# Kernel optimization log

Measured on AMD Instinct MI355X. Metric: run time of the kernel, lower is better.

## Reference

```python
import jax, jax.numpy as jnp
import numpy as np

N_COMP = 8
N_BASIS = 16
N_FEATURES = 64
N_CAT = 8
N_CONT = 56
N_UNIQUE = 100
BATCH = 32768
T0, T1 = 0.0, 10.0
SEP = 1e-3  # constants.MIN_TRANSITION_POINT_SEP
SIGNS = np.array([1.0, -1.0, 1.0, -1.0, 1.0, -1.0, 1.0, -1.0], dtype=np.float32)
CONT_IDX = np.arange(N_CONT)
CAT_IDX = np.arange(N_CONT, N_FEATURES)


def _offset():
    # torch_inverse_softplus(avg_interval_per_feature)
    v = (T1 - T0) / N_COMP / (N_FEATURES + 1)
    return float(np.log(np.exp(v) - 1.0))


def setup_inputs():
    key = jax.random.key(0)
    ks = jax.random.split(key, 11)
    off = _offset()
    B = jax.random.normal(ks[0], (BATCH, N_CONT, N_BASIS), jnp.float32)
    codes = jax.random.randint(ks[1], (BATCH, N_CAT), 0, N_UNIQUE)
    B_cat = jax.nn.one_hot(codes, N_UNIQUE, dtype=jnp.float32).reshape(BATCH, N_CAT * N_UNIQUE)
    Wh = jax.random.normal(ks[2], (N_BASIS, N_CONT, N_COMP), jnp.float32) + off
    Wh_cat = jax.random.normal(ks[3], (N_CAT, N_UNIQUE, N_COMP), jnp.float32) + off
    bh = jax.random.normal(ks[4], (N_COMP,), jnp.float32) + off
    Wv = jax.random.normal(ks[5], (N_BASIS, N_CONT, N_COMP), jnp.float32)
    Wv_cat = jax.random.normal(ks[6], (N_CAT, N_UNIQUE, N_COMP), jnp.float32)
    bv = jax.random.normal(ks[7], (N_COMP,), jnp.float32)
    Wic = jax.random.normal(ks[8], (N_BASIS, N_CONT, 1), jnp.float32)
    Wic_cat = jax.random.normal(ks[9], (N_CAT, N_UNIQUE, 1), jnp.float32)
    bic = jax.random.normal(ks[10], (1,), jnp.float32)
    return {"B": B, "B_cat": B_cat, "Wh": Wh, "Wh_cat": Wh_cat, "bh": bh,
            "Wv": Wv, "Wv_cat": Wv_cat, "bv": bv,
            "Wic": Wic, "Wic_cat": Wic_cat, "bic": bic}


def _calculate_gams(B, B_cat, W, W_cat, bias, positive):
    # continuous: per-feature small matmul  (b,i,k) x (k,i,c) -> (b,c,i)
    cont = jnp.einsum('bik,kic->bci', B, W)
    # categorical: one-hot gather expressed as blockwise matmul  (b,f,n) x (f,n,c) -> (b,c,f)
    cat = jnp.einsum('bfn,fnc->bcf', B_cat.reshape(B.shape[0], N_CAT, N_UNIQUE), W_cat)
    c = W.shape[2]
    out = jnp.zeros((B.shape[0], c, N_FEATURES + 1), dtype=B.dtype)
    out = out.at[:, :, CONT_IDX].set(cont)
    out = out.at[:, :, CAT_IDX].set(cat)
    out = out.at[:, :, -1].set(bias[None, :])
    return jax.nn.softplus(out) if positive else out


def reference(B, B_cat, Wh, Wh_cat, bh, Wv, Wv_cat, bv, Wic, Wic_cat, bic):
    H = _calculate_gams(B, B_cat, Wh, Wh_cat, bh, True)      # (b, n_comp, n_feat+1)
    V = _calculate_gams(B, B_cat, Wv, Wv_cat, bv, True)      # (b, n_comp, n_feat+1)
    IC = _calculate_gams(B, B_cat, Wic, Wic_cat, bic, False)  # (b, 1, n_feat+1)
    b = B.shape[0]
    signs = jnp.asarray(SIGNS)
    h_sum = H.sum(-1)   # (b, n_comp) per-segment horizontal increments
    v_sum = V.sum(-1)
    sep = SEP * jnp.arange(1, N_COMP + 1, dtype=B.dtype)
    # sequential cumulative build == prefix sums over the composition axis
    t = jnp.concatenate([jnp.full((b, 1), T0, B.dtype),
                         T0 + jnp.cumsum(h_sum, axis=1) + sep], axis=1)  # (b, n_comp+1)
    x0 = IC.sum(-1)     # (b, 1)
    x = jnp.concatenate([x0, x0 + jnp.cumsum(signs * v_sum, axis=1)], axis=1)
    # bounded composition: clamp the last horizontal coordinate
    t = t.at[:, -1].set(jnp.maximum(t[:, -2] + SEP, T1))
    return jnp.stack([t, x], axis=-1)  # (b, n_comp+1, 2)
```

## Files before the change

### kernel.cpp

```cpp
#include <hip/hip_runtime.h>

#define NCOMP 8
#define NCONT 56
#define NCAT 8
#define NU 100
#define NROWS 32768
#define SEPC 1e-3f
#define T1F 10.0f

typedef __fp16 f16x2 __attribute__((ext_vector_type(2)));
typedef _Float16 h2arith __attribute__((ext_vector_type(2)));

#define HSTRIDE 17
#define ICSTRIDE 3

union H8 { f16x2 h2[4]; float4 f4; };

__device__ __forceinline__ float sp(float x) {
    return 0.69314718f * __builtin_amdgcn_logf(1.0f + __builtin_amdgcn_exp2f(x * 1.44269504f));
}

__device__ __forceinline__ f16x2 pkrtz(float a, float b) {
    return __builtin_amdgcn_cvt_pkrtz(a, b);
}

__device__ __forceinline__ float fdot2(f16x2 a, f16x2 b, float c) {
    return __builtin_amdgcn_fdot2(a, b, c, false);
}

__device__ __forceinline__ h2arith h2shfl_xor(h2arith v, int off) {
    int i = __builtin_bit_cast(int, v);
    i = __shfl_xor(i, off, 64);
    return __builtin_bit_cast(h2arith, i);
}

__global__ __launch_bounds__(1024, 8) void tpm_kernel(
    const float* __restrict__ B, const float* __restrict__ Bcat,
    const float* __restrict__ Wh, const float* __restrict__ Whc, const float* __restrict__ bh,
    const float* __restrict__ Wv, const float* __restrict__ Wvc, const float* __restrict__ bv,
    const float* __restrict__ Wic, const float* __restrict__ Wicc, const float* __restrict__ bic,
    float* __restrict__ out)
{
    __shared__ float4 sH4[NCONT * HSTRIDE];
    __shared__ float4 sV4[NCONT * HSTRIDE];
    __shared__ float4 sIC4[NCONT * ICSTRIDE];
    __shared__ float2 sBias[NCOMP];
    __shared__ float  sBic;
    __shared__ int    sCode[16][NCAT];

    const int tid = threadIdx.x;

    if (tid < 896) {
        int icp = tid % 448, t = tid / 448;
        int i = icp >> 3, c = icp & 7;
        const float* gh = Wh + (size_t)(8 * t) * 448 + icp;
        const float* gv = Wv + (size_t)(8 * t) * 448 + icp;
        H8 uh, uv;
#pragma unroll
        for (int p = 0; p < 4; ++p) {
            uh.h2[p] = pkrtz(gh[(2 * p) * 448], gh[(2 * p + 1) * 448]);
            uv.h2[p] = pkrtz(gv[(2 * p) * 448], gv[(2 * p + 1) * 448]);
        }
        sH4[i * HSTRIDE + c * 2 + t] = uh.f4;
        sV4[i * HSTRIDE + c * 2 + t] = uv.f4;
    }
    if (tid < 112) {
        int i = tid % 56, t = tid / 56;
        const float* gi = Wic + (size_t)(8 * t) * 56 + i;
        H8 u;
#pragma unroll
        for (int p = 0; p < 4; ++p)
            u.h2[p] = pkrtz(gi[(2 * p) * 56], gi[(2 * p + 1) * 56]);
        sIC4[i * ICSTRIDE + t] = u.f4;
    }
    if (tid < NCOMP) sBias[tid] = make_float2(sp(bh[tid]), sp(bv[tid]));
    if (tid == NCOMP) sBic = bic[0];
    __syncthreads();

    const int lane = tid & 63;
    const int widx = tid >> 6;
    const int gw = (blockIdx.x << 4) + widx;
    const int nw = gridDim.x << 4;

    const float4* pH = sH4 + lane * HSTRIDE;
    const float4* pV = sV4 + lane * HSTRIDE;
    const float4* pIC = sIC4 + lane * ICSTRIDE;

    for (int r = gw; r < NROWS; r += nw) {
        const float4* pc = (const float4*)(Bcat + (size_t)r * 800);
#pragma unroll
        for (int it = 0; it < 4; ++it) {
            int v = it * 64 + lane;
            if (it < 3 || v < 200) {
                float4 q = pc[v];
                float n = (float)(4 * v);
                float s = q.x * (n + 1.0f) + q.y * (n + 2.0f) + q.z * (n + 3.0f) + q.w * (n + 4.0f);
                if (s > 0.5f) {
                    int p = (int)s - 1;
                    int f = p / NU;
                    sCode[widx][f] = p - f * NU;
                }
            }
        }
        __threadfence_block();

        float h[NCOMP], w[NCOMP], ic;
        if (lane < NCONT) {
            const float4* pB = (const float4*)(B + (size_t)r * 896 + lane * 16);
            float4 b0 = pB[0], b1 = pB[1], b2 = pB[2], b3 = pB[3];
            f16x2 bb[8];
            bb[0] = pkrtz(b0.x, b0.y);
            bb[1] = pkrtz(b0.z, b0.w);
            bb[2] = pkrtz(b1.x, b1.y);
            bb[3] = pkrtz(b1.z, b1.w);
            bb[4] = pkrtz(b2.x, b2.y);
            bb[5] = pkrtz(b2.z, b2.w);
            bb[6] = pkrtz(b3.x, b3.y);
            bb[7] = pkrtz(b3.z, b3.w);
#pragma unroll
            for (int c = 0; c < NCOMP; ++c) {
                H8 u0, u1, v0, v1;
                u0.f4 = pH[2 * c]; u1.f4 = pH[2 * c + 1];
                v0.f4 = pV[2 * c]; v1.f4 = pV[2 * c + 1];
                float ah = 0.0f, av = 0.0f;
#pragma unroll
                for (int p = 0; p < 4; ++p) {
                    ah = fdot2(bb[p], u0.h2[p], ah);
                    av = fdot2(bb[p], v0.h2[p], av);
                }
#pragma unroll
                for (int p = 0; p < 4; ++p) {
                    ah = fdot2(bb[4 + p], u1.h2[p], ah);
                    av = fdot2(bb[4 + p], v1.h2[p], av);
                }
                h[c] = ah; w[c] = av;
            }
            H8 i0, i1;
            i0.f4 = pIC[0]; i1.f4 = pIC[1];
            float ai = 0.0f;
#pragma unroll
            for (int p = 0; p < 4; ++p) ai = fdot2(bb[p], i0.h2[p], ai);
#pragma unroll
            for (int p = 0; p < 4; ++p) ai = fdot2(bb[4 + p], i1.h2[p], ai);
            ic = ai;
        } else {
            int f = lane - NCONT;
            int g = f * NU + sCode[widx][f];
            const float4* qh = (const float4*)(Whc + g * 8);
            const float4* qv = (const float4*)(Wvc + g * 8);
            float4 a0 = qh[0], a1 = qh[1];
            float4 c0 = qv[0], c1 = qv[1];
            h[0] = a0.x; h[1] = a0.y; h[2] = a0.z; h[3] = a0.w;
            h[4] = a1.x; h[5] = a1.y; h[6] = a1.z; h[7] = a1.w;
            w[0] = c0.x; w[1] = c0.y; w[2] = c0.z; w[3] = c0.w;
            w[4] = c1.x; w[5] = c1.y; w[6] = c1.z; w[7] = c1.w;
            ic = Wicc[g];
        }

        h2arith hw[NCOMP];
#pragma unroll
        for (int c = 0; c < NCOMP; ++c)
            hw[c] = __builtin_bit_cast(h2arith, pkrtz(sp(h[c]), sp(w[c])));

#pragma unroll
        for (int off = 32; off >= 1; off >>= 1) {
#pragma unroll
            for (int c = 0; c < NCOMP; ++c)
                hw[c] = hw[c] + h2shfl_xor(hw[c], off);
            ic += __shfl_xor(ic, off, 64);
        }

        if (lane < 9) {
            int m = (lane == 8) ? 7 : lane;
            float tj = SEPC * (float)lane;
            float xj = ic + sBic;
#pragma unroll
            for (int c = 0; c < NCOMP; ++c) {
                float2 bb2 = sBias[c];
                if (c < m)    tj += (float)hw[c][0] + bb2.x;
                if (c < lane) {
                    float vv = (float)hw[c][1] + bb2.y;
                    xj += (c & 1) ? -vv : vv;
                }
            }
            if (lane == 8) tj = fmaxf(tj, T1F);
            float2 o; o.x = tj; o.y = xj;
            ((float2*)out)[(size_t)r * 9 + lane] = o;
        }
    }
}

extern "C" void kernel_launch(void* const* d_in, const int* in_sizes, int n_in,
                              void* d_out, int out_size, void* d_ws, size_t ws_size,
                              hipStream_t stream) {
    (void)in_sizes; (void)n_in; (void)out_size; (void)d_ws; (void)ws_size;
    const float* B    = (const float*)d_in[0];
    const float* Bcat = (const float*)d_in[1];
    const float* Wh   = (const float*)d_in[2];
    const float* Whc  = (const float*)d_in[3];
    const float* bh   = (const float*)d_in[4];
    const float* Wv   = (const float*)d_in[5];
    const float* Wvc  = (const float*)d_in[6];
    const float* bv   = (const float*)d_in[7];
    const float* Wic  = (const float*)d_in[8];
    const float* Wicc = (const float*)d_in[9];
    const float* bic  = (const float*)d_in[10];
    float* out = (float*)d_out;

    hipLaunchKernelGGL(tpm_kernel, dim3(512), dim3(1024), 0, stream,
                       B, Bcat, Wh, Whc, bh, Wv, Wvc, bv, Wic, Wicc, bic, out);
}
```

Baseline: 275.0 us.

## Process eight rows per wave with 16-lane row groups and fused weight LDS

Remaps work so each wave handles eight rows at once. Each 16-lane group owns two rows and loops over features in four passes, with each weight load from LDS reused for both rows. Softplus is accumulated per lane before a 16-wide shuffle reduction, replacing the 64-wide one, and the H/V/IC weights share one shared-memory array. Categorical decoding of all eight rows is done up front, and the grid is halved so each wave handles exactly one batch of eight rows. The per-thread register load rises, and the launch bound drops to four blocks per multiprocessor, which may lower occupancy.

```diff
diff --git a/kernel.cpp b/kernel.cpp
--- a/kernel.cpp
+++ b/kernel.cpp
@@ -11,8 +11,7 @@
 typedef __fp16 f16x2 __attribute__((ext_vector_type(2)));
 typedef _Float16 h2arith __attribute__((ext_vector_type(2)));
 
-#define HSTRIDE 17
-#define ICSTRIDE 3
+#define FSTRIDE 35
 
 union H8 { f16x2 h2[4]; float4 f4; };
 
@@ -34,19 +33,17 @@
     return __builtin_bit_cast(h2arith, i);
 }
 
-__global__ __launch_bounds__(1024, 8) void tpm_kernel(
+__global__ __launch_bounds__(1024, 4) void tpm_kernel(
     const float* __restrict__ B, const float* __restrict__ Bcat,
     const float* __restrict__ Wh, const float* __restrict__ Whc, const float* __restrict__ bh,
     const float* __restrict__ Wv, const float* __restrict__ Wvc, const float* __restrict__ bv,
     const float* __restrict__ Wic, const float* __restrict__ Wicc, const float* __restrict__ bic,
     float* __restrict__ out)
 {
-    __shared__ float4 sH4[NCONT * HSTRIDE];
-    __shared__ float4 sV4[NCONT * HSTRIDE];
-    __shared__ float4 sIC4[NCONT * ICSTRIDE];
+    __shared__ float4 sW[NCONT * FSTRIDE];
     __shared__ float2 sBias[NCOMP];
     __shared__ float  sBic;
-    __shared__ int    sCode[16][NCAT];
+    __shared__ int    sCode[16][8][NCAT];
 
     const int tid = threadIdx.x;
 
@@ -61,8 +58,8 @@
             uh.h2[p] = pkrtz(gh[(2 * p) * 448], gh[(2 * p + 1) * 448]);
             uv.h2[p] = pkrtz(gv[(2 * p) * 448], gv[(2 * p + 1) * 448]);
         }
-        sH4[i * HSTRIDE + c * 2 + t] = uh.f4;
-        sV4[i * HSTRIDE + c * 2 + t] = uv.f4;
+        sW[i * FSTRIDE + 2 * c + t] = uh.f4;
+        sW[i * FSTRIDE + 16 + 2 * c + t] = uv.f4;
     }
     if (tid < 112) {
         int i = tid % 56, t = tid / 56;
@@ -71,7 +68,7 @@
 #pragma unroll
         for (int p = 0; p < 4; ++p)
             u.h2[p] = pkrtz(gi[(2 * p) * 56], gi[(2 * p + 1) * 56]);
-        sIC4[i * ICSTRIDE + t] = u.f4;
+        sW[i * FSTRIDE + 32 + t] = u.f4;
     }
     if (tid < NCOMP) sBias[tid] = make_float2(sp(bh[tid]), sp(bv[tid]));
     if (tid == NCOMP) sBic = bic[0];
@@ -79,114 +76,159 @@
 
     const int lane = tid & 63;
     const int widx = tid >> 6;
-    const int gw = (blockIdx.x << 4) + widx;
-    const int nw = gridDim.x << 4;
-
-    const float4* pH = sH4 + lane * HSTRIDE;
-    const float4* pV = sV4 + lane * HSTRIDE;
-    const float4* pIC = sIC4 + lane * ICSTRIDE;
-
-    for (int r = gw; r < NROWS; r += nw) {
-        const float4* pc = (const float4*)(Bcat + (size_t)r * 800);
-#pragma unroll
-        for (int it = 0; it < 4; ++it) {
-            int v = it * 64 + lane;
-            if (it < 3 || v < 200) {
-                float4 q = pc[v];
-                float n = (float)(4 * v);
-                float s = q.x * (n + 1.0f) + q.y * (n + 2.0f) + q.z * (n + 3.0f) + q.w * (n + 4.0f);
-                if (s > 0.5f) {
-                    int p = (int)s - 1;
-                    int f = p / NU;
-                    sCode[widx][f] = p - f * NU;
-                }
-            }
-        }
-        __threadfence_block();
-
-        float h[NCOMP], w[NCOMP], ic;
-        if (lane < NCONT) {
-            const float4* pB = (const float4*)(B + (size_t)r * 896 + lane * 16);
+    const int s = lane & 15;
+    const int g = lane >> 4;
+    const int R0 = ((blockIdx.x << 4) + widx) << 3;
+    const int rA = R0 + g;
+    const int rB = R0 + 4 + g;
+
+    {
+        const float4* pc = (const float4*)(Bcat + (size_t)R0 * 800);
+#pragma unroll
+        for (int it = 0; it < 25; ++it) {
+            int idx = it * 64 + lane;
+            int row = idx / 200;
+            int pos = idx - row * 200;
+            float4 q = pc[row * 200 + pos];
+            float n = (float)(4 * pos);
+            float sc = q.x * (n + 1.0f) + q.y * (n + 2.0f) + q.z * (n + 3.0f) + q.w * (n + 4.0f);
+            if (sc > 0.5f) {
+                int p = (int)sc - 1;
+                int f = p / NU;
+                sCode[widx][row][f] = p - f * NU;
+            }
+        }
+    }
+    __threadfence_block();
+
+    float shA[NCOMP], swA[NCOMP], shB[NCOMP], swB[NCOMP];
+    float icA = 0.0f, icB = 0.0f;
+#pragma unroll
+    for (int c = 0; c < NCOMP; ++c) { shA[c] = swA[c] = shB[c] = swB[c] = 0.0f; }
+
+#pragma unroll 1
+    for (int j = 0; j < 4; ++j) {
+        int f = s + 16 * j;
+        if (f < NCONT) {
+            const float4* pA = (const float4*)(B + (size_t)rA * 896 + f * 16);
+            const float4* pB = (const float4*)(B + (size_t)rB * 896 + f * 16);
+            float4 a0 = pA[0], a1 = pA[1], a2 = pA[2], a3 = pA[3];
             float4 b0 = pB[0], b1 = pB[1], b2 = pB[2], b3 = pB[3];
-            f16x2 bb[8];
-            bb[0] = pkrtz(b0.x, b0.y);
-            bb[1] = pkrtz(b0.z, b0.w);
-            bb[2] = pkrtz(b1.x, b1.y);
-            bb[3] = pkrtz(b1.z, b1.w);
-            bb[4] = pkrtz(b2.x, b2.y);
-            bb[5] = pkrtz(b2.z, b2.w);
-            bb[6] = pkrtz(b3.x, b3.y);
-            bb[7] = pkrtz(b3.z, b3.w);
+            f16x2 baA[8], baB[8];
+            baA[0] = pkrtz(a0.x, a0.y); baA[1] = pkrtz(a0.z, a0.w);
+            baA[2] = pkrtz(a1.x, a1.y); baA[3] = pkrtz(a1.z, a1.w);
+            baA[4] = pkrtz(a2.x, a2.y); baA[5] = pkrtz(a2.z, a2.w);
+            baA[6] = pkrtz(a3.x, a3.y); baA[7] = pkrtz(a3.z, a3.w);
+            baB[0] = pkrtz(b0.x, b0.y); baB[1] = pkrtz(b0.z, b0.w);
+            baB[2] = pkrtz(b1.x, b1.y); baB[3] = pkrtz(b1.z, b1.w);
+            baB[4] = pkrtz(b2.x, b2.y); baB[5] = pkrtz(b2.z, b2.w);
+            baB[6] = pkrtz(b3.x, b3.y); baB[7] = pkrtz(b3.z, b3.w);
+
+            const float4* pw = sW + f * FSTRIDE;
 #pragma unroll
             for (int c = 0; c < NCOMP; ++c) {
                 H8 u0, u1, v0, v1;
-                u0.f4 = pH[2 * c]; u1.f4 = pH[2 * c + 1];
-                v0.f4 = pV[2 * c]; v1.f4 = pV[2 * c + 1];
-                float ah = 0.0f, av = 0.0f;
-#pragma unroll
-                for (int p = 0; p < 4; ++p) {
-                    ah = fdot2(bb[p], u0.h2[p], ah);
-                    av = fdot2(bb[p], v0.h2[p], av);
-                }
-#pragma unroll
-                for (int p = 0; p < 4; ++p) {
-                    ah = fdot2(bb[4 + p], u1.h2[p], ah);
-                    av = fdot2(bb[4 + p], v1.h2[p], av);
-                }
-                h[c] = ah; w[c] = av;
-            }
-            H8 i0, i1;
-            i0.f4 = pIC[0]; i1.f4 = pIC[1];
-            float ai = 0.0f;
-#pragma unroll
-            for (int p = 0; p < 4; ++p) ai = fdot2(bb[p], i0.h2[p], ai);
-#pragma unroll
-            for (int p = 0; p < 4; ++p) ai = fdot2(bb[4 + p], i1.h2[p], ai);
-            ic = ai;
+                u0.f4 = pw[2 * c];      u1.f4 = pw[2 * c + 1];
+                v0.f4 = pw[16 + 2 * c]; v1.f4 = pw[17 + 2 * c];
+                float hA = 0.0f, hB = 0.0f, vA = 0.0f, vB = 0.0f;
+#pragma unroll
+                for (int p = 0; p < 4; ++p) {
+                    hA = fdot2(baA[p], u0.h2[p], hA);
+                    hB = fdot2(baB[p], u0.h2[p], hB);
+                    vA = fdot2(baA[p], v0.h2[p], vA);
+                    vB = fdot2(baB[p], v0.h2[p], vB);
+                }
+#pragma unroll
+                for (int p = 0; p < 4; ++p) {
+                    hA = fdot2(baA[4 + p], u1.h2[p], hA);
+                    hB = fdot2(baB[4 + p], u1.h2[p], hB);
+                    vA = fdot2(baA[4 + p], v1.h2[p], vA);
+                    vB = fdot2(baB[4 + p], v1.h2[p], vB);
+                }
+                shA[c] += sp(hA); shB[c] += sp(hB);
+                swA[c] += sp(vA); swB[c] += sp(vB);
+            }
+            {
+                H8 i0, i1;
+                i0.f4 = pw[32]; i1.f4 = pw[33];
+                float iA = 0.0f, iB = 0.0f;
+#pragma unroll
+                for (int p = 0; p < 4; ++p) {
+                    iA = fdot2(baA[p], i0.h2[p], iA);
+                    iB = fdot2(baB[p], i0.h2[p], iB);
+                }
+#pragma unroll
+                for (int p = 0; p < 4; ++p) {
+                    iA = fdot2(baA[4 + p], i1.h2[p], iA);
+                    iB = fdot2(baB[4 + p], i1.h2[p], iB);
+                }
+                icA += iA; icB += iB;
+            }
         } else {
-            int f = lane - NCONT;
-            int g = f * NU + sCode[widx][f];
-            const float4* qh = (const float4*)(Whc + g * 8);
-            const float4* qv = (const float4*)(Wvc + g * 8);
-            float4 a0 = qh[0], a1 = qh[1];
-            float4 c0 = qv[0], c1 = qv[1];
-            h[0] = a0.x; h[1] = a0.y; h[2] = a0.z; h[3] = a0.w;
-            h[4] = a1.x; h[5] = a1.y; h[6] = a1.z; h[7] = a1.w;
-            w[0] = c0.x; w[1] = c0.y; w[2] = c0.z; w[3] = c0.w;
-            w[4] = c1.x; w[5] = c1.y; w[6] = c1.z; w[7] = c1.w;
-            ic = Wicc[g];
-        }
-
-        h2arith hw[NCOMP];
-#pragma unroll
-        for (int c = 0; c < NCOMP; ++c)
-            hw[c] = __builtin_bit_cast(h2arith, pkrtz(sp(h[c]), sp(w[c])));
-
-#pragma unroll
-        for (int off = 32; off >= 1; off >>= 1) {
-#pragma unroll
-            for (int c = 0; c < NCOMP; ++c)
-                hw[c] = hw[c] + h2shfl_xor(hw[c], off);
-            ic += __shfl_xor(ic, off, 64);
-        }
-
-        if (lane < 9) {
-            int m = (lane == 8) ? 7 : lane;
-            float tj = SEPC * (float)lane;
-            float xj = ic + sBic;
-#pragma unroll
-            for (int c = 0; c < NCOMP; ++c) {
-                float2 bb2 = sBias[c];
-                if (c < m)    tj += (float)hw[c][0] + bb2.x;
-                if (c < lane) {
-                    float vv = (float)hw[c][1] + bb2.y;
-                    xj += (c & 1) ? -vv : vv;
-                }
-            }
-            if (lane == 8) tj = fmaxf(tj, T1F);
-            float2 o; o.x = tj; o.y = xj;
-            ((float2*)out)[(size_t)r * 9 + lane] = o;
-        }
+            int fi = s - 8;
+            int cA = sCode[widx][g][fi];
+            int cB = sCode[widx][4 + g][fi];
+            int gA = fi * NU + cA;
+            int gB = fi * NU + cB;
+            const float4* qhA = (const float4*)(Whc + gA * 8);
+            const float4* qvA = (const float4*)(Wvc + gA * 8);
+            const float4* qhB = (const float4*)(Whc + gB * 8);
+            const float4* qvB = (const float4*)(Wvc + gB * 8);
+            float4 h0 = qhA[0], h1 = qhA[1], v0 = qvA[0], v1 = qvA[1];
+            shA[0] += sp(h0.x); shA[1] += sp(h0.y); shA[2] += sp(h0.z); shA[3] += sp(h0.w);
+            shA[4] += sp(h1.x); shA[5] += sp(h1.y); shA[6] += sp(h1.z); shA[7] += sp(h1.w);
+            swA[0] += sp(v0.x); swA[1] += sp(v0.y); swA[2] += sp(v0.z); swA[3] += sp(v0.w);
+            swA[4] += sp(v1.x); swA[5] += sp(v1.y); swA[6] += sp(v1.z); swA[7] += sp(v1.w);
+            icA += Wicc[gA];
+            float4 h2 = qhB[0], h3 = qhB[1], v2 = qvB[0], v3 = qvB[1];
+            shB[0] += sp(h2.x); shB[1] += sp(h2.y); shB[2] += sp(h2.z); shB[3] += sp(h2.w);
+            shB[4] += sp(h3.x); shB[5] += sp(h3.y); shB[6] += sp(h3.z); shB[7] += sp(h3.w);
+            swB[0] += sp(v2.x); swB[1] += sp(v2.y); swB[2] += sp(v2.z); swB[3] += sp(v2.w);
+            swB[4] += sp(v3.x); swB[5] += sp(v3.y); swB[6] += sp(v3.z); swB[7] += sp(v3.w);
+            icB += Wicc[gB];
+        }
+    }
+
+    h2arith hwA[NCOMP], hwB[NCOMP];
+#pragma unroll
+    for (int c = 0; c < NCOMP; ++c) {
+        hwA[c] = __builtin_bit_cast(h2arith, pkrtz(shA[c], swA[c]));
+        hwB[c] = __builtin_bit_cast(h2arith, pkrtz(shB[c], swB[c]));
+    }
+#pragma unroll
+    for (int off = 8; off >= 1; off >>= 1) {
+#pragma unroll
+        for (int c = 0; c < NCOMP; ++c) {
+            hwA[c] = hwA[c] + h2shfl_xor(hwA[c], off);
+            hwB[c] = hwB[c] + h2shfl_xor(hwB[c], off);
+        }
+        icA += __shfl_xor(icA, off, 64);
+        icB += __shfl_xor(icB, off, 64);
+    }
+
+    if (s < 9) {
+        int m = (s == 9 - 1) ? 7 : s;
+        float tA = SEPC * (float)s, tB = tA;
+        float xA = icA + sBic, xB = icB + sBic;
+#pragma unroll
+        for (int c = 0; c < NCOMP; ++c) {
+            float2 bb2 = sBias[c];
+            if (c < m) {
+                tA += (float)hwA[c][0] + bb2.x;
+                tB += (float)hwB[c][0] + bb2.x;
+            }
+            if (c < s) {
+                float vA = (float)hwA[c][1] + bb2.y;
+                float vB = (float)hwB[c][1] + bb2.y;
+                xA += (c & 1) ? -vA : vA;
+                xB += (c & 1) ? -vB : vB;
+            }
+        }
+        if (s == 8) { tA = fmaxf(tA, T1F); tB = fmaxf(tB, T1F); }
+        float2 oA; oA.x = tA; oA.y = xA;
+        float2 oB; oB.x = tB; oB.y = xB;
+        ((float2*)out)[(size_t)rA * 9 + s] = oA;
+        ((float2*)out)[(size_t)rB * 9 + s] = oB;
     }
 }
 
@@ -207,6 +249,6 @@
     const float* bic  = (const float*)d_in[10];
     float* out = (float*)d_out;
 
-    hipLaunchKernelGGL(tpm_kernel, dim3(512), dim3(1024), 0, stream,
+    hipLaunchKernelGGL(tpm_kernel, dim3(256), dim3(1024), 0, stream,
                        B, Bcat, Wh, Whc, bh, Wv, Wvc, bv, Wic, Wicc, bic, out);
 }
```

New measurement: 263.0 us. -4.4%, faster.
